# Kernel tuning notes

Measured on AMD Instinct MI355X. Metric: run time of the kernel, lower is better.

Reference implementation:

```python
import jax, jax.numpy as jnp
import numpy as np

DIM = 128
NUM_HEADS = 4
WINDOW = (7, 7)


def _rel_pos_index(wh, ww):
    h = jnp.arange(wh)
    w = jnp.arange(ww)
    idx = jnp.stack(jnp.meshgrid(w, h, indexing='ij'))  # (2, wh, ww)
    flat = idx.reshape(2, -1)                           # (2, n)
    rel = flat[:, :, None] - flat[:, None, :]           # (2, n, n)
    rel = jnp.transpose(rel, (1, 2, 0))                 # (n, n, 2)
    rel = rel.at[:, :, 0].add(wh - 1)
    rel = rel.at[:, :, 1].add(ww - 1)
    rel = rel.at[:, :, 0].multiply(2 * ww - 1)
    return jnp.sum(rel, -1)                             # (n, n)


def setup_inputs() -> dict:
    key = jax.random.key(0)
    ks = jax.random.split(key, 7)
    batch, n, c = 4096, WINDOW[0] * WINDOW[1], DIM
    nw = 64  # windows per image; batch % nw == 0
    return {
        'inputs': jax.random.normal(ks[0], (batch, n, c), jnp.float32),
        'mask': jax.random.normal(ks[1], (nw, n, n), jnp.float32),
        'qkv_w': jax.random.normal(ks[2], (c, 3 * c), jnp.float32) * 0.02,
        'qkv_b': jax.random.normal(ks[3], (3 * c,), jnp.float32) * 0.02,
        'proj_w': jax.random.normal(ks[4], (c, c), jnp.float32) * 0.02,
        'proj_b': jax.random.normal(ks[5], (c,), jnp.float32) * 0.02,
        'rpbt': jax.random.normal(ks[6], ((2 * WINDOW[0] - 1) * (2 * WINDOW[1] - 1), NUM_HEADS), jnp.float32) * 0.02,
    }


def reference(inputs, mask, qkv_w, qkv_b, proj_w, proj_b, rpbt):
    batch, n, c = inputs.shape
    head_dim = DIM // NUM_HEADS
    qkv = inputs @ qkv_w + qkv_b                       # (B, n, 3C)
    qkv = qkv.reshape(batch, n, 3, NUM_HEADS, head_dim)
    qkv = jnp.transpose(qkv, (2, 0, 3, 1, 4))          # (3, B, H, n, d)
    q, k, v = qkv[0], qkv[1], qkv[2]
    q = q * head_dim ** -0.5
    att = jnp.einsum('bhqd,bhkd->bhqk', q, k)          # (B, H, n, n)
    rel_idx = _rel_pos_index(*WINDOW).reshape(-1)
    bias = rpbt[rel_idx].reshape(n, n, NUM_HEADS)      # gather
    att = att + jnp.transpose(bias, (2, 0, 1))[None]   # (B, H, n, n)
    nw = mask.shape[0]
    att = att.reshape(batch // nw, nw, NUM_HEADS, n, n)
    att = att + mask[None, :, None]
    att = att.reshape(batch, NUM_HEADS, n, n)
    att = jax.nn.softmax(att, axis=-1)
    x = jnp.einsum('bhqk,bhkd->bhqd', att, v)          # (B, H, n, d)
    x = jnp.transpose(x, (0, 2, 1, 3)).reshape(batch, n, c)
    return x @ proj_w + proj_b
```

## Files before the change

### kernel.cpp

```cpp
#include <hip/hip_runtime.h>

typedef __bf16 bf16x8 __attribute__((ext_vector_type(8)));
typedef float f32x4 __attribute__((ext_vector_type(4)));
typedef float f32x16 __attribute__((ext_vector_type(16)));
typedef unsigned short us4 __attribute__((ext_vector_type(4)));
typedef unsigned int u32x2 __attribute__((ext_vector_type(2)));

#define SCALE 0.17677669529663687f

__device__ __forceinline__ unsigned short f2bf(float f) {
    __bf16 h = (__bf16)f;
    return __builtin_bit_cast(unsigned short, h);
}
__device__ __forceinline__ unsigned cvtpk(float lo, float hi) {
    unsigned r;
    asm("v_cvt_pk_bf16_f32 %0, %1, %2" : "=v"(r) : "v"(lo), "v"(hi));
    return r;
}

__global__ void wa_prep(const float* __restrict__ qkv_w, const float* __restrict__ proj_w,
                        const float* __restrict__ rpbt, const float* __restrict__ mask,
                        unsigned short* __restrict__ wq2, unsigned short* __restrict__ wp2,
                        float* __restrict__ tab, int use_bm) {
    int idx = blockIdx.x * 256 + threadIdx.x;
    if (idx < 49152) {
        int c2 = idx / 3072, rem = idx % 3072;
        int n = rem >> 3, j = rem & 7;
        int k = c2 * 8 + j;
        float v = qkv_w[k * 384 + n];
        if (n < 128) v *= SCALE;
        wq2[idx] = f2bf(v);
    } else if (idx < 65536) {
        int t = idx - 49152;
        int c2 = t >> 10, rem = t & 1023;
        int n = rem >> 3, j = rem & 7;
        int k = c2 * 8 + j;
        wp2[t] = f2bf(proj_w[k * 128 + n]);
    } else {
        int j = idx - 65536;
        if (use_bm) {
            if (j < 64 * 4 * 49 * 64) {
                int k = j & 63; int t = j >> 6; int q = t % 49; t /= 49;
                int h = t & 3, w = t >> 2;
                float v = 0.f;
                if (k < 49) {
                    int rel = (q / 7 - k / 7 + 6) * 13 + (q % 7 - k % 7 + 6);
                    v = rpbt[rel * 4 + h] + mask[w * 2401 + q * 49 + k];
                }
                tab[j] = v;
            }
        } else {
            if (j < 4 * 49 * 64) {
                int k = j & 63; int t = j >> 6; int q = t % 49; int h = t / 49;
                float v = 0.f;
                if (k < 49) {
                    int rel = (q / 7 - k / 7 + 6) * 13 + (q % 7 - k % 7 + 6);
                    v = rpbt[rel * 4 + h];
                }
                tab[j] = v;
            }
        }
    }
}

__global__ __launch_bounds__(512, 6) void wa_main(
    const float* __restrict__ x, const float* __restrict__ mask,
    const float* __restrict__ qkv_b, const float* __restrict__ proj_b,
    const unsigned short* __restrict__ wq2, const unsigned short* __restrict__ wp2,
    const float* __restrict__ tab, int use_bm, float* __restrict__ out)
{
    __shared__ __align__(16) char smem[49152];
    char* const Qs = smem;
    char* const Ks = smem + 16384;
    char* const Cx = smem + 32768;

    const int tid  = threadIdx.x;
    const int wv   = tid >> 6;
    const int lane = tid & 63;
    const int l31  = lane & 31;
    const int hi   = lane >> 5;
    const int b    = blockIdx.x;

    {
        const float* xp = x + (size_t)b * 6272;
        for (int i = tid; i < 1568; i += 512) {
            int row = i >> 5;
            int cb  = (i & 31) * 8;
            f32x4 v = *reinterpret_cast<const f32x4*>(xp + i * 4);
            u32x2 sv;
            sv[0] = cvtpk(v[0], v[1]);
            sv[1] = cvtpk(v[2], v[3]);
            *reinterpret_cast<u32x2*>(Cx + row * 256 + (cb ^ ((row & 7) << 4))) = sv;
        }
        u32x2 z = (u32x2)0u;
        for (int i = tid; i < 480; i += 512) {
            int row = 49 + (i >> 5);
            int cb  = (i & 31) * 8;
            *reinterpret_cast<u32x2*>(Cx + row * 256 + (cb ^ ((row & 7) << 4))) = z;
        }
    }
    __syncthreads();

    {
        const int rt = wv >> 2, c4 = wv & 3;
        const int arow = rt * 32 + l31;

        #pragma unroll 1
        for (int t = 0; t < 2; ++t) {
            const int colg = t * 128 + c4 * 32 + l31;
            f32x16 acc;
            #pragma unroll
            for (int i = 0; i < 16; ++i) acc[i] = 0.f;
            __builtin_amdgcn_s_setprio(1);
            #pragma unroll
            for (int kk = 0; kk < 8; ++kk) {
                bf16x8 af = *reinterpret_cast<const bf16x8*>(
                    Cx + arow * 256 + ((kk * 32 + hi * 16) ^ ((arow & 7) << 4)));
                bf16x8 bw = *reinterpret_cast<const bf16x8*>(
                    wq2 + ((kk * 2 + hi) * 384 + colg) * 8);
                acc = __builtin_amdgcn_mfma_f32_32x32x16_bf16(af, bw, acc, 0, 0, 0);
            }
            __builtin_amdgcn_s_setprio(0);
            float bv = qkv_b[colg] * (t == 0 ? SCALE : 1.0f);
            char* dst = (t == 0 ? Qs : Ks);
            #pragma unroll
            for (int r = 0; r < 16; ++r) {
                int row = rt * 32 + (r & 3) + 8 * (r >> 2) + 4 * hi;
                *reinterpret_cast<unsigned short*>(
                    dst + c4 * 4096 + row * 64 + ((l31 * 2) ^ ((row & 3) << 4))) = f2bf(acc[r] + bv);
            }
        }
        f32x16 avv;
        #pragma unroll
        for (int i = 0; i < 16; ++i) avv[i] = 0.f;
        {
            const int colg = 256 + c4 * 32 + l31;
            __builtin_amdgcn_s_setprio(1);
            #pragma unroll
            for (int kk = 0; kk < 8; ++kk) {
                bf16x8 af = *reinterpret_cast<const bf16x8*>(
                    Cx + arow * 256 + ((kk * 32 + hi * 16) ^ ((arow & 7) << 4)));
                bf16x8 bw = *reinterpret_cast<const bf16x8*>(
                    wq2 + ((kk * 2 + hi) * 384 + colg) * 8);
                avv = __builtin_amdgcn_mfma_f32_32x32x16_bf16(af, bw, avv, 0, 0, 0);
            }
            __builtin_amdgcn_s_setprio(0);
        }
        __syncthreads();
        {
            float bvv = qkv_b[256 + c4 * 32 + l31];
            #pragma unroll
            for (int g = 0; g < 4; ++g) {
                int tok0 = rt * 32 + 8 * g + 4 * hi;
                u32x2 pv;
                pv[0] = cvtpk(avv[g * 4 + 0] + bvv, avv[g * 4 + 1] + bvv);
                pv[1] = cvtpk(avv[g * 4 + 2] + bvv, avv[g * 4 + 3] + bvv);
                *reinterpret_cast<u32x2*>(
                    Cx + c4 * 4096 + l31 * 128 + ((tok0 * 2) ^ ((l31 & 7) << 4))) = pv;
            }
        }
    }
    __syncthreads();

    {
        const int h2 = wv >> 1, qh = wv & 1;
        const int q  = qh * 32 + l31;

        f32x16 S0, S1;
        #pragma unroll
        for (int i = 0; i < 16; ++i) { S0[i] = 0.f; S1[i] = 0.f; }
        __builtin_amdgcn_s_setprio(1);
        #pragma unroll
        for (int s = 0; s < 2; ++s) {
            const int off = s * 32 + hi * 16;
            bf16x8 qf = *reinterpret_cast<const bf16x8*>(
                Qs + h2 * 4096 + q * 64 + (off ^ ((q & 3) << 4)));
            bf16x8 k0 = *reinterpret_cast<const bf16x8*>(
                Ks + h2 * 4096 + l31 * 64 + (off ^ ((l31 & 3) << 4)));
            bf16x8 k1 = *reinterpret_cast<const bf16x8*>(
                Ks + h2 * 4096 + (32 + l31) * 64 + (off ^ ((l31 & 3) << 4)));
            S0 = __builtin_amdgcn_mfma_f32_32x32x16_bf16(k0, qf, S0, 0, 0, 0);
            S1 = __builtin_amdgcn_mfma_f32_32x32x16_bf16(k1, qf, S1, 0, 0, 0);
        }
        __builtin_amdgcn_s_setprio(0);

        const float* tp = tab + (size_t)(use_bm ? ((b & 63) * 4 + h2) : h2) * (49 * 64);
        const float* mp = mask + (size_t)(b & 63) * 2401;
        const bool qv = q < 49;
        const int qc = qv ? q : 48;
        const float* trow = tp + qc * 64;

        float mx = -1e30f;
        #pragma unroll
        for (int g = 0; g < 4; ++g) {
            f32x4 t0 = *reinterpret_cast<const f32x4*>(trow + g * 8 + hi * 4);
            f32x4 t1 = *reinterpret_cast<const f32x4*>(trow + 32 + g * 8 + hi * 4);
            #pragma unroll
            for (int e = 0; e < 4; ++e) {
                float v0 = S0[g * 4 + e] + t0[e];
                float v1 = S1[g * 4 + e] + t1[e];
                if (!use_bm) {
                    v0 += mp[qc * 49 + g * 8 + hi * 4 + e];
                    int k1i = 32 + g * 8 + hi * 4 + e;
                    if (k1i < 49) v1 += mp[qc * 49 + k1i];
                }
                v0 = qv ? v0 : -1e30f;
                v1 = (qv && (g * 8 + hi * 4 + e) < 17) ? v1 : -1e30f;
                S0[g * 4 + e] = v0;  mx = fmaxf(mx, v0);
                S1[g * 4 + e] = v1;  mx = fmaxf(mx, v1);
            }
        }
        mx = fmaxf(mx, __shfl_xor(mx, 32));
        float sum = 0.f;
        #pragma unroll
        for (int i = 0; i < 16; ++i) {
            float e0 = __expf(S0[i] - mx);
            float e1 = __expf(S1[i] - mx);
            S0[i] = e0; S1[i] = e1;
            sum += e0 + e1;
        }
        sum += __shfl_xor(sum, 32);
        float ri = __builtin_amdgcn_rcpf(sum);

        unsigned pp[2][4][2];
        #pragma unroll
        for (int g = 0; g < 4; ++g) {
            pp[0][g][0] = cvtpk(S0[g * 4 + 0] * ri, S0[g * 4 + 1] * ri);
            pp[0][g][1] = cvtpk(S0[g * 4 + 2] * ri, S0[g * 4 + 3] * ri);
            pp[1][g][0] = cvtpk(S1[g * 4 + 0] * ri, S1[g * 4 + 1] * ri);
            pp[1][g][1] = cvtpk(S1[g * 4 + 2] * ri, S1[g * 4 + 3] * ri);
        }

        f32x16 X;
        #pragma unroll
        for (int i = 0; i < 16; ++i) X[i] = 0.f;
        const bool lo = (hi == 0);
        __builtin_amdgcn_s_setprio(1);
        #pragma unroll
        for (int s = 0; s < 4; ++s) {
            const int kt = s >> 1, u = (s & 1) * 2;
            unsigned a0 = pp[kt][u][0],     a1 = pp[kt][u][1];
            unsigned b0 = pp[kt][u + 1][0], b1 = pp[kt][u + 1][1];
            unsigned sa0 = (unsigned)__shfl_xor((int)a0, 32);
            unsigned sa1 = (unsigned)__shfl_xor((int)a1, 32);
            unsigned sb0 = (unsigned)__shfl_xor((int)b0, 32);
            unsigned sb1 = (unsigned)__shfl_xor((int)b1, 32);
            union { unsigned u4[4]; bf16x8 v; } A;
            A.u4[0] = lo ? a0  : sb0;
            A.u4[1] = lo ? a1  : sb1;
            A.u4[2] = lo ? sa0 : b0;
            A.u4[3] = lo ? sa1 : b1;
            bf16x8 Bf = *reinterpret_cast<const bf16x8*>(
                Cx + h2 * 4096 + l31 * 128 + ((s * 32 + hi * 16) ^ ((l31 & 7) << 4)));
            X = __builtin_amdgcn_mfma_f32_32x32x16_bf16(A.v, Bf, X, 0, 0, 0);
        }
        __builtin_amdgcn_s_setprio(0);
        __syncthreads();
        #pragma unroll
        for (int r = 0; r < 16; ++r) {
            int row = qh * 32 + (r & 3) + 8 * (r >> 2) + 4 * hi;
            int col = h2 * 32 + l31;
            *reinterpret_cast<unsigned short*>(
                Qs + row * 256 + ((col * 2) ^ ((row & 7) << 4))) = f2bf(X[r]);
        }
    }
    __syncthreads();

    {
        const int prt = wv >> 2, pct = wv & 3;
        const int xrow = prt * 32 + l31;
        f32x16 o;
        #pragma unroll
        for (int i = 0; i < 16; ++i) o[i] = 0.f;
        __builtin_amdgcn_s_setprio(1);
        #pragma unroll
        for (int kk = 0; kk < 8; ++kk) {
            bf16x8 af = *reinterpret_cast<const bf16x8*>(
                Qs + xrow * 256 + ((kk * 32 + hi * 16) ^ ((xrow & 7) << 4)));
            bf16x8 bw = *reinterpret_cast<const bf16x8*>(
                wp2 + ((kk * 2 + hi) * 128 + pct * 32 + l31) * 8);
            o = __builtin_amdgcn_mfma_f32_32x32x16_bf16(af, bw, o, 0, 0, 0);
        }
        __builtin_amdgcn_s_setprio(0);
        float pb = proj_b[pct * 32 + l31];
        float* op = out + (size_t)b * 6272 + pct * 32 + l31;
        #pragma unroll
        for (int r = 0; r < 16; ++r) {
            int row = prt * 32 + (r & 3) + 8 * (r >> 2) + 4 * hi;
            if (row < 49) op[row * 128] = o[r] + pb;
        }
    }
}

extern "C" void kernel_launch(void* const* d_in, const int* in_sizes, int n_in,
                              void* d_out, int out_size, void* d_ws, size_t ws_size,
                              hipStream_t stream) {
    const float* x      = (const float*)d_in[0];
    const float* mask   = (const float*)d_in[1];
    const float* qkv_w  = (const float*)d_in[2];
    const float* qkv_b  = (const float*)d_in[3];
    const float* proj_w = (const float*)d_in[4];
    const float* proj_b = (const float*)d_in[5];
    const float* rpbt   = (const float*)d_in[6];
    float* out = (float*)d_out;

    unsigned short* wq2 = (unsigned short*)d_ws;
    unsigned short* wp2 = (unsigned short*)((char*)d_ws + 98304);
    float*          tab = (float*)((char*)d_ws + 131072);

    const size_t needed_big = 131072 + (size_t)64 * 4 * 49 * 64 * 4;
    int use_bm = (ws_size >= needed_big) ? 1 : 0;
    int total  = 65536 + (use_bm ? 64 * 4 * 49 * 64 : 4 * 49 * 64);

    wa_prep<<<(total + 255) / 256, 256, 0, stream>>>(qkv_w, proj_w, rpbt, mask, wq2, wp2, tab, use_bm);
    wa_main<<<4096, 512, 0, stream>>>(x, mask, qkv_b, proj_b, wq2, wp2, tab, use_bm, out);
}
```

Baseline: 106.7 us.

## Transpose QK projection output and use padded LDS rows for vectorized packed stores

The Q/K projection MFMA swaps operands so each lane holds consecutive head-dim values, and the results go to padded LDS rows (72-byte stride) as packed bf16 pairs instead of scalar 16-bit swizzled stores. The attention output is likewise computed transposed and written as packed u32x2 into padded 264-byte rows for the projection stage. Q bias pre-scaling moves into the prep kernel so it can be loaded as f32x4. The aim is fewer LDS store instructions and no XOR swizzle arithmetic, at the cost of more shared memory per block, which may lower occupancy.

```diff
diff --git a/kernel.cpp b/kernel.cpp
--- a/kernel.cpp
+++ b/kernel.cpp
@@ -20,8 +20,9 @@
 
 __global__ void wa_prep(const float* __restrict__ qkv_w, const float* __restrict__ proj_w,
                         const float* __restrict__ rpbt, const float* __restrict__ mask,
+                        const float* __restrict__ qkv_b,
                         unsigned short* __restrict__ wq2, unsigned short* __restrict__ wp2,
-                        float* __restrict__ tab, int use_bm) {
+                        float* __restrict__ tab, float* __restrict__ qb2, int use_bm) {
     int idx = blockIdx.x * 256 + threadIdx.x;
     if (idx < 49152) {
         int c2 = idx / 3072, rem = idx % 3072;
@@ -38,8 +39,9 @@
         wp2[t] = f2bf(proj_w[k * 128 + n]);
     } else {
         int j = idx - 65536;
-        if (use_bm) {
-            if (j < 64 * 4 * 49 * 64) {
+        const int tabN = use_bm ? 64 * 4 * 49 * 64 : 4 * 49 * 64;
+        if (j < tabN) {
+            if (use_bm) {
                 int k = j & 63; int t = j >> 6; int q = t % 49; t /= 49;
                 int h = t & 3, w = t >> 2;
                 float v = 0.f;
@@ -48,9 +50,7 @@
                     v = rpbt[rel * 4 + h] + mask[w * 2401 + q * 49 + k];
                 }
                 tab[j] = v;
-            }
-        } else {
-            if (j < 4 * 49 * 64) {
+            } else {
                 int k = j & 63; int t = j >> 6; int q = t % 49; int h = t / 49;
                 float v = 0.f;
                 if (k < 49) {
@@ -59,20 +59,23 @@
                 }
                 tab[j] = v;
             }
+        } else if (j < tabN + 384) {
+            int c = j - tabN;
+            qb2[c] = qkv_b[c] * (c < 128 ? SCALE : 1.0f);
         }
     }
 }
 
 __global__ __launch_bounds__(512, 6) void wa_main(
     const float* __restrict__ x, const float* __restrict__ mask,
-    const float* __restrict__ qkv_b, const float* __restrict__ proj_b,
+    const float* __restrict__ qb2, const float* __restrict__ proj_b,
     const unsigned short* __restrict__ wq2, const unsigned short* __restrict__ wp2,
     const float* __restrict__ tab, int use_bm, float* __restrict__ out)
 {
-    __shared__ __align__(16) char smem[49152];
-    char* const Qs = smem;
-    char* const Ks = smem + 16384;
-    char* const Cx = smem + 32768;
+    __shared__ __align__(16) char smem[53248];
+    char* const Qp = smem;
+    char* const Kp = smem + 18432;
+    char* const Cx = smem + 36864;
 
     const int tid  = threadIdx.x;
     const int wv   = tid >> 6;
@@ -103,7 +106,7 @@
 
     {
         const int rt = wv >> 2, c4 = wv & 3;
-        const int arow = rt * 32 + l31;
+        const int tokrow = rt * 32 + l31;
 
         #pragma unroll 1
         for (int t = 0; t < 2; ++t) {
@@ -114,20 +117,22 @@
             __builtin_amdgcn_s_setprio(1);
             #pragma unroll
             for (int kk = 0; kk < 8; ++kk) {
-                bf16x8 af = *reinterpret_cast<const bf16x8*>(
-                    Cx + arow * 256 + ((kk * 32 + hi * 16) ^ ((arow & 7) << 4)));
-                bf16x8 bw = *reinterpret_cast<const bf16x8*>(
+                bf16x8 bx = *reinterpret_cast<const bf16x8*>(
+                    Cx + tokrow * 256 + ((kk * 32 + hi * 16) ^ ((tokrow & 7) << 4)));
+                bf16x8 aw = *reinterpret_cast<const bf16x8*>(
                     wq2 + ((kk * 2 + hi) * 384 + colg) * 8);
-                acc = __builtin_amdgcn_mfma_f32_32x32x16_bf16(af, bw, acc, 0, 0, 0);
+                acc = __builtin_amdgcn_mfma_f32_32x32x16_bf16(aw, bx, acc, 0, 0, 0);
             }
             __builtin_amdgcn_s_setprio(0);
-            float bv = qkv_b[colg] * (t == 0 ? SCALE : 1.0f);
-            char* dst = (t == 0 ? Qs : Ks);
-            #pragma unroll
-            for (int r = 0; r < 16; ++r) {
-                int row = rt * 32 + (r & 3) + 8 * (r >> 2) + 4 * hi;
-                *reinterpret_cast<unsigned short*>(
-                    dst + c4 * 4096 + row * 64 + ((l31 * 2) ^ ((row & 3) << 4))) = f2bf(acc[r] + bv);
+            char* dst = (t == 0 ? Qp : Kp) + c4 * 4608 + tokrow * 72;
+            const float* qb = qb2 + t * 128 + c4 * 32;
+            #pragma unroll
+            for (int g = 0; g < 4; ++g) {
+                f32x4 bq = *reinterpret_cast<const f32x4*>(qb + 8 * g + 4 * hi);
+                u32x2 pv;
+                pv[0] = cvtpk(acc[4 * g + 0] + bq[0], acc[4 * g + 1] + bq[1]);
+                pv[1] = cvtpk(acc[4 * g + 2] + bq[2], acc[4 * g + 3] + bq[3]);
+                *reinterpret_cast<u32x2*>(dst + 16 * g + 8 * hi) = pv;
             }
         }
         f32x16 avv;
@@ -139,7 +144,7 @@
             #pragma unroll
             for (int kk = 0; kk < 8; ++kk) {
                 bf16x8 af = *reinterpret_cast<const bf16x8*>(
-                    Cx + arow * 256 + ((kk * 32 + hi * 16) ^ ((arow & 7) << 4)));
+                    Cx + tokrow * 256 + ((kk * 32 + hi * 16) ^ ((tokrow & 7) << 4)));
                 bf16x8 bw = *reinterpret_cast<const bf16x8*>(
                     wq2 + ((kk * 2 + hi) * 384 + colg) * 8);
                 avv = __builtin_amdgcn_mfma_f32_32x32x16_bf16(af, bw, avv, 0, 0, 0);
@@ -148,7 +153,7 @@
         }
         __syncthreads();
         {
-            float bvv = qkv_b[256 + c4 * 32 + l31];
+            float bvv = qb2[256 + c4 * 32 + l31];
             #pragma unroll
             for (int g = 0; g < 4; ++g) {
                 int tok0 = rt * 32 + 8 * g + 4 * hi;
@@ -173,12 +178,9 @@
         #pragma unroll
         for (int s = 0; s < 2; ++s) {
             const int off = s * 32 + hi * 16;
-            bf16x8 qf = *reinterpret_cast<const bf16x8*>(
-                Qs + h2 * 4096 + q * 64 + (off ^ ((q & 3) << 4)));
-            bf16x8 k0 = *reinterpret_cast<const bf16x8*>(
-                Ks + h2 * 4096 + l31 * 64 + (off ^ ((l31 & 3) << 4)));
-            bf16x8 k1 = *reinterpret_cast<const bf16x8*>(
-                Ks + h2 * 4096 + (32 + l31) * 64 + (off ^ ((l31 & 3) << 4)));
+            bf16x8 qf = *reinterpret_cast<const bf16x8*>(Qp + h2 * 4608 + q * 72 + off);
+            bf16x8 k0 = *reinterpret_cast<const bf16x8*>(Kp + h2 * 4608 + l31 * 72 + off);
+            bf16x8 k1 = *reinterpret_cast<const bf16x8*>(Kp + h2 * 4608 + (32 + l31) * 72 + off);
             S0 = __builtin_amdgcn_mfma_f32_32x32x16_bf16(k0, qf, S0, 0, 0, 0);
             S1 = __builtin_amdgcn_mfma_f32_32x32x16_bf16(k1, qf, S1, 0, 0, 0);
         }
@@ -250,18 +252,21 @@
             A.u4[1] = lo ? a1  : sb1;
             A.u4[2] = lo ? sa0 : b0;
             A.u4[3] = lo ? sa1 : b1;
-            bf16x8 Bf = *reinterpret_cast<const bf16x8*>(
+            bf16x8 Vf = *reinterpret_cast<const bf16x8*>(
                 Cx + h2 * 4096 + l31 * 128 + ((s * 32 + hi * 16) ^ ((l31 & 7) << 4)));
-            X = __builtin_amdgcn_mfma_f32_32x32x16_bf16(A.v, Bf, X, 0, 0, 0);
+            X = __builtin_amdgcn_mfma_f32_32x32x16_bf16(Vf, A.v, X, 0, 0, 0);
         }
         __builtin_amdgcn_s_setprio(0);
         __syncthreads();
-        #pragma unroll
-        for (int r = 0; r < 16; ++r) {
-            int row = qh * 32 + (r & 3) + 8 * (r >> 2) + 4 * hi;
-            int col = h2 * 32 + l31;
-            *reinterpret_cast<unsigned short*>(
-                Qs + row * 256 + ((col * 2) ^ ((row & 7) << 4))) = f2bf(X[r]);
+        {
+            char* xd = Qp + q * 264 + h2 * 64;
+            #pragma unroll
+            for (int g = 0; g < 4; ++g) {
+                u32x2 pv;
+                pv[0] = cvtpk(X[4 * g + 0], X[4 * g + 1]);
+                pv[1] = cvtpk(X[4 * g + 2], X[4 * g + 3]);
+                *reinterpret_cast<u32x2*>(xd + 16 * g + 8 * hi) = pv;
+            }
         }
     }
     __syncthreads();
@@ -276,7 +281,7 @@
         #pragma unroll
         for (int kk = 0; kk < 8; ++kk) {
             bf16x8 af = *reinterpret_cast<const bf16x8*>(
-                Qs + xrow * 256 + ((kk * 32 + hi * 16) ^ ((xrow & 7) << 4)));
+                Qp + xrow * 264 + kk * 32 + hi * 16);
             bf16x8 bw = *reinterpret_cast<const bf16x8*>(
                 wp2 + ((kk * 2 + hi) * 128 + pct * 32 + l31) * 8);
             o = __builtin_amdgcn_mfma_f32_32x32x16_bf16(af, bw, o, 0, 0, 0);
@@ -304,14 +309,19 @@
     const float* rpbt   = (const float*)d_in[6];
     float* out = (float*)d_out;
 
+    const size_t tab_big = (size_t)64 * 4 * 49 * 64;
+    const size_t tab_sm  = (size_t)4 * 49 * 64;
+    const size_t needed_big = 131072 + (tab_big + 384) * 4;
+    int use_bm = (ws_size >= needed_big) ? 1 : 0;
+    const size_t tabN = use_bm ? tab_big : tab_sm;
+
     unsigned short* wq2 = (unsigned short*)d_ws;
     unsigned short* wp2 = (unsigned short*)((char*)d_ws + 98304);
     float*          tab = (float*)((char*)d_ws + 131072);
-
-    const size_t needed_big = 131072 + (size_t)64 * 4 * 49 * 64 * 4;
-    int use_bm = (ws_size >= needed_big) ? 1 : 0;
-    int total  = 65536 + (use_bm ? 64 * 4 * 49 * 64 : 4 * 49 * 64);
-
-    wa_prep<<<(total + 255) / 256, 256, 0, stream>>>(qkv_w, proj_w, rpbt, mask, wq2, wp2, tab, use_bm);
-    wa_main<<<4096, 512, 0, stream>>>(x, mask, qkv_b, proj_b, wq2, wp2, tab, use_bm, out);
-}
+    float*          qb2 = (float*)((char*)d_ws + 131072 + tabN * 4);
+
+    int total = 65536 + (int)tabN + 384;
+    wa_prep<<<(total + 255) / 256, 256, 0, stream>>>(qkv_w, proj_w, rpbt, mask, qkv_b,
+                                                     wq2, wp2, tab, qb2, use_bm);
+    wa_main<<<4096, 512, 0, stream>>>(x, mask, qb2, proj_b, wq2, wp2, tab, use_bm, out);
+}
```

Result: slower. 121.1 us (+13.5%).
